# Kernel tuning notes

Measured on AMD Instinct MI355X. Metric: run time of the kernel, lower is better.

The kernel has to match this reference:

```python
import jax, jax.numpy as jnp
import numpy as np

M, N, P, T = 8000, 63, 64, 5


def setup_inputs() -> dict:
    key = jax.random.key(0)
    ks = jax.random.split(key, 19)
    sn = (1.0 / N) ** 0.5
    sp = (1.0 / P) ** 0.5
    f32 = jnp.float32
    return {
        "A": jax.random.normal(ks[0], (1, M, N), f32),
        "b": jax.random.normal(ks[1], (1, M), f32),
        "c": jax.random.normal(ks[2], (1, N), f32),
        "theta1r": sn * jax.random.normal(ks[3], (P, N + 1), f32),
        "theta1c": sn * jax.random.normal(ks[4], (P, N + 1), f32),
        "theta2rr": sp * jax.random.normal(ks[5], (P, P), f32),
        "theta2rc": sp * jax.random.normal(ks[6], (P, P), f32),
        "theta2cr": sp * jax.random.normal(ks[7], (P, P), f32),
        "theta3rr": sp * jax.random.normal(ks[8], (P, P), f32),
        "theta3rc": sp * jax.random.normal(ks[9], (P, P), f32),
        "theta3cr": sp * jax.random.normal(ks[10], (P, P), f32),
        "theta4rr": sp * jax.random.normal(ks[11], (P,), f32),
        "theta4rc": sp * jax.random.normal(ks[12], (P,), f32),
        "theta4cr": sp * jax.random.normal(ks[13], (P,), f32),
        "theta6r": sp * jax.random.normal(ks[14], (P, P), f32),
        "theta6c": sp * jax.random.normal(ks[15], (P, P), f32),
        "theta7": sp * jax.random.normal(ks[16], (P, P), f32),
        "W8": 0.05 * jax.random.normal(ks[17], (2, 2 * P), f32),
        "b8": 0.05 * jax.random.normal(ks[18], (2,), f32),
        "z": 7,
    }


def reference(A, b, c, theta1r, theta1c, theta2rr, theta2rc, theta2cr,
              theta3rr, theta3rc, theta3cr, theta4rr, theta4rc, theta4cr,
              theta6r, theta6c, theta7, W8, b8, z):
    relu = jax.nn.relu
    m, n = A.shape[1], A.shape[2]
    p = theta1r.shape[0]
    # raw node features: row node v -> [A[v,:], b[v]]; column node m -> [c, 0]
    Fr_raw = jnp.concatenate([A[0], b[0][:, None]], axis=1)        # (m, n+1)
    fc_raw = jnp.concatenate([c[0], jnp.zeros((1,), A.dtype)])     # (n+1,)
    Fr = Fr_raw / jnp.linalg.norm(Fr_raw, axis=1, keepdims=True)   # f(v), v < m
    fc = fc_raw / jnp.linalg.norm(fc_raw)                          # f(m)
    # edge weights w(v,u) = f(v).f(u) are detached in the original (float(...data))
    Frd = jax.lax.stop_gradient(Fr)
    fcd = jax.lax.stop_gradient(fc)
    Wrr = Frd @ Frd.T                                              # (m, m)
    dg = jnp.diagonal(Wrr)
    srr_pos = relu(Wrr).sum(axis=1) - relu(dg)                     # sum over u != v
    srr_neg = relu(-Wrr).sum(axis=1) - relu(-dg)
    wrc = Frd @ fcd                                                # (m,) = w(v, m)
    # identity: sum_u relu(t4 * w_u) = relu(t4) * sum_u relu(w_u) + relu(-t4) * sum_u relu(-w_u)
    Srr = relu(theta4rr)[:, None] * srr_pos[None, :] + relu(-theta4rr)[:, None] * srr_neg[None, :]
    Src = relu(theta4rc)[:, None] * relu(wrc)[None, :] + relu(-theta4rc)[:, None] * relu(-wrc)[None, :]
    scr = relu(theta4cr) * relu(wrc).sum() + relu(-theta4cr) * relu(-wrc).sum()
    edge_r = theta3rr @ Srr + theta3rc @ Src                       # (p, m), constant over t
    edge_c = theta3cr @ scr                                        # (p,)
    fz = Fr[z]                                                     # z < m: row node feature
    t1r = theta1r @ fz                                             # (p,)
    t1c = theta1c @ fz
    # mu init (p, m+1) = [[Ab^T, c0^T]; 0]; split into row columns / column node
    mu_r0 = jnp.zeros((p, m), A.dtype).at[: n + 1].set(Fr_raw.T)
    mu_c0 = jnp.zeros((p,), A.dtype).at[: n + 1].set(fc_raw)

    def step(carry, _):
        mu_r, mu_c = carry
        # row nodes: term2rr uses old mu[:, v]; term2rc uses old mu[:, m]
        new_r = relu(t1r[:, None] + theta2rr @ mu_r + (theta2rc @ mu_c)[:, None] + edge_r)
        # column node updated last within a sweep -> sees updated row embeddings
        new_c = relu(t1c + theta2cr @ new_r.sum(axis=1) + edge_c)
        return (new_r, new_c), None

    (mu_r, mu_c), _ = jax.lax.scan(step, (mu_r0, mu_c0), None, length=T)
    term6 = theta6r @ mu_r.sum(axis=1) + theta6c @ mu_c            # (p,)
    term7 = theta7 @ mu_r[:, z]                                    # (p,)
    feat = jax.nn.sigmoid(jnp.concatenate([term6, term7]))         # (2p,)
    return (feat @ W8.T + b8)[None, :]                             # (1, 2)
```

## Files before the change

kernel.cpp:

```cpp
#include <hip/hip_runtime.h>
#include <math.h>

typedef __attribute__((ext_vector_type(8))) short short8;
typedef __attribute__((ext_vector_type(4))) float f32x4;

#define WS_SPART 0
#define WS_GPART 262144
#define WS_WPART 294912
#define WS_CPART 295936
#define WS_T1R   336896
#define WS_T1C   336960
#define WS_AL    337024
#define WS_BE    337088
#define WS_GA    337152
#define WS_DE    337216
#define WS_ECP   337280
#define WS_ECN   337344
#define WS_W     337408
#define WS_MUZ   337472
#define WS_WSUM  337536
#define WS_RNORM 337600
#define WS_R2H   345792
#define WS_R2L   347840
#define WS_CNT   349888
#define WS_FH    380928
#define WS_FL    643072

#define NBLK 125

__device__ __forceinline__ float waveReduceSum(float v) {
#pragma unroll
    for (int m = 32; m >= 1; m >>= 1) v += __shfl_xor(v, m, 64);
    return v;
}
__device__ __forceinline__ unsigned short f2bf(float f) {
    unsigned int u = __float_as_uint(f);
    unsigned int r = (u + 0x7fffu + ((u >> 16) & 1u)) >> 16;
    return (unsigned short)r;
}
__device__ __forceinline__ float bf2f(unsigned short h) {
    return __uint_as_float(((unsigned int)h) << 16);
}

__device__ __forceinline__ float sum32_coherent(const float* base) {
    float v[32];
#pragma unroll
    for (int i = 0; i < 32; i++)
        asm volatile("global_load_dword %0, %1, off sc0 sc1"
                     : "=v"(v[i]) : "v"(base + i * 256));
    asm volatile("s_waitcnt vmcnt(0)" ::: "memory");
    __builtin_amdgcn_sched_barrier(0);
    float s = 0.f;
#pragma unroll
    for (int i = 0; i < 32; i++) s += v[i];
    return s;
}

__global__ __launch_bounds__(256) void k_fr(
    const float* __restrict__ A, const float* __restrict__ b, const float* __restrict__ c,
    const float* __restrict__ th1r, const float* __restrict__ th1c,
    const float* __restrict__ th2rr, const float* __restrict__ th2rc,
    const float* __restrict__ th3rr, const float* __restrict__ th3rc, const float* __restrict__ th3cr,
    const float* __restrict__ th4rr, const float* __restrict__ th4rc, const float* __restrict__ th4cr,
    const int* __restrict__ zp,
    unsigned short* __restrict__ Fh, unsigned short* __restrict__ Fl,
    unsigned short* __restrict__ R2H, unsigned short* __restrict__ R2L,
    float* __restrict__ ws)
{
    int tid = threadIdx.x, lane = tid & 63, wid = tid >> 6;

    if (blockIdx.x == 512) {
        __shared__ float fcraw[64], fz[64], sh4a[64], sh4b[64];
        int p = lane;
        int z = zp[0];
        float cv = (p < 63) ? c[p] : 0.f;
        fcraw[p] = cv;
        float av = (p < 63) ? A[z * 63 + p] : b[z];
        float s2 = waveReduceSum(av * av);
        fz[p] = av * rsqrtf(s2);
        __syncthreads();

        float t1 = 0.f, t2 = 0.f, w0 = 0.f;
#pragma unroll 8
        for (int k = 0; k < 64; k++) {
            t1 += th1r[p * 64 + k] * fz[k];
            t2 += th1c[p * 64 + k] * fz[k];
            w0 += th2rc[p * 64 + k] * fcraw[k];
        }
        ws[WS_T1R + p] = t1;
        ws[WS_T1C + p] = t2;
        ws[WS_W + p] = t1 + w0;

        sh4a[p] = th4rr[p];
        sh4b[p] = th4rc[p];
        __syncthreads();
        float a = 0.f, bb = 0.f, g = 0.f, d = 0.f;
#pragma unroll 8
        for (int k = 0; k < 64; k++) {
            float t4 = sh4a[k];
            a  += th3rr[p * 64 + k] * fmaxf(t4, 0.f);
            bb += th3rr[p * 64 + k] * fmaxf(-t4, 0.f);
            float t5 = sh4b[k];
            g  += th3rc[p * 64 + k] * fmaxf(t5, 0.f);
            d  += th3rc[p * 64 + k] * fmaxf(-t5, 0.f);
        }
        ws[WS_AL + p] = a; ws[WS_BE + p] = bb;
        ws[WS_GA + p] = g; ws[WS_DE + p] = d;
        __syncthreads();
        sh4a[p] = th4cr[p];
        __syncthreads();
        float e1 = 0.f, e2 = 0.f;
#pragma unroll 8
        for (int k = 0; k < 64; k++) {
            float t6 = sh4a[k];
            e1 += th3cr[p * 64 + k] * fmaxf(t6, 0.f);
            e2 += th3cr[p * 64 + k] * fmaxf(-t6, 0.f);
        }
        ws[WS_ECP + p] = e1; ws[WS_ECN + p] = e2;

        if (tid < 16) ((int*)(ws + WS_CNT))[tid] = 0;
        if (tid < 192) {
#pragma unroll
            for (int t5 = 0; t5 < 5; t5++)
                ws[WS_CPART + t5 * 8192 + 8000 + tid] = 0.f;
        }

#pragma unroll
        for (int i = 0; i < 16; i++) {
            int idx = tid * 16 + i;
            float f = th2rr[idx];
            unsigned short h = f2bf(f);
            R2H[idx] = h;
            R2L[idx] = f2bf(f - bf2f(h));
        }
        return;
    }

    __shared__ float gsh[64];
    __shared__ float wsh2[2];
    if (tid < 64) gsh[tid] = 0.f;
    if (tid < 2) wsh2[tid] = 0.f;
    __syncthreads();

    float cv = (lane < 63) ? c[lane] : 0.f;
    float cn2 = waveReduceSum(cv * cv);
    float fcnl = cv * rsqrtf(cn2);

    int r0 = blockIdx.x * 16 + wid * 4;
    float gl = 0.f, lp = 0.f, ln = 0.f;
#pragma unroll
    for (int i = 0; i < 4; i++) {
        int r = r0 + i;
        if (r < 8000) {
            float val = (lane < 63) ? A[r * 63 + lane] : b[r];
            float s2 = waveReduceSum(val * val);
            float f = val * rsqrtf(s2);
            unsigned short h = f2bf(f);
            Fh[r * 64 + lane] = h;
            Fl[r * 64 + lane] = f2bf(f - bf2f(h));
            gl += f;
            float w = waveReduceSum(f * fcnl);
            if (lane == 0) {
                ws[WS_RNORM + r] = sqrtf(s2);
                lp += fmaxf(w, 0.f); ln += fmaxf(-w, 0.f);
            }
        } else {
            Fh[r * 64 + lane] = 0;
            Fl[r * 64 + lane] = 0;
        }
    }
    atomicAdd(&gsh[lane], gl);
    if (lane == 0) { atomicAdd(&wsh2[0], lp); atomicAdd(&wsh2[1], ln); }
    __syncthreads();
    if (tid < 64) ws[WS_GPART + blockIdx.x * 64 + tid] = gsh[tid];
    if (tid == 64) ws[WS_WPART + blockIdx.x * 2 + 0] = wsh2[0];
    if (tid == 65) ws[WS_WPART + blockIdx.x * 2 + 1] = wsh2[1];
}

__global__ __launch_bounds__(256) void k_gram(
    const unsigned short* __restrict__ Fh, float* __restrict__ ws)
{
    int tid = threadIdx.x, lane = tid & 63, wid = tid >> 6;
    int m = lane & 15, quad = lane >> 4;
    int vbase = blockIdx.x * 256 + wid * 64;

    short8 AH[8];
#pragma unroll
    for (int pt = 0; pt < 4; pt++)
#pragma unroll
        for (int q = 0; q < 2; q++)
            AH[pt * 2 + q] = *(const short8*)(Fh + (vbase + pt * 16 + m) * 64 + q * 32 + quad * 8);

    float srr[16];
#pragma unroll
    for (int i = 0; i < 16; i++) srr[i] = 0.f;

    const int y = blockIdx.y;
    const int boff = m * 64 + quad * 8;
    short8 B0[2], B1[2];
#pragma unroll
    for (int q = 0; q < 2; q++)
        B0[q] = *(const short8*)(Fh + y * 16 * 64 + boff + q * 32);

#pragma unroll 1
    for (int k2 = 0; k2 < 8; k2++) {
        int jB1 = y + 32 * (2 * k2 + 1);
#pragma unroll
        for (int q = 0; q < 2; q++)
            B1[q] = *(const short8*)(Fh + jB1 * 16 * 64 + boff + q * 32);
#pragma unroll
        for (int pt = 0; pt < 4; pt++) {
            f32x4 a = {0.f, 0.f, 0.f, 0.f};
            a = __builtin_amdgcn_mfma_f32_16x16x32_bf16(AH[pt * 2 + 0], B0[0], a, 0, 0, 0);
            a = __builtin_amdgcn_mfma_f32_16x16x32_bf16(AH[pt * 2 + 1], B0[1], a, 0, 0, 0);
#pragma unroll
            for (int r = 0; r < 4; r++) srr[pt * 4 + r] += fmaxf(a[r], 0.f);
        }
        if (k2 < 7) {
            int jB0 = y + 32 * (2 * k2 + 2);
#pragma unroll
            for (int q = 0; q < 2; q++)
                B0[q] = *(const short8*)(Fh + jB0 * 16 * 64 + boff + q * 32);
        }
#pragma unroll
        for (int pt = 0; pt < 4; pt++) {
            f32x4 a = {0.f, 0.f, 0.f, 0.f};
            a = __builtin_amdgcn_mfma_f32_16x16x32_bf16(AH[pt * 2 + 0], B1[0], a, 0, 0, 0);
            a = __builtin_amdgcn_mfma_f32_16x16x32_bf16(AH[pt * 2 + 1], B1[1], a, 0, 0, 0);
#pragma unroll
            for (int r = 0; r < 4; r++) srr[pt * 4 + r] += fmaxf(a[r], 0.f);
        }
    }
#pragma unroll
    for (int pt = 0; pt < 4; pt++)
#pragma unroll
        for (int r = 0; r < 4; r++) {
            float s = srr[pt * 4 + r];
            s += __shfl_xor(s, 1, 64); s += __shfl_xor(s, 2, 64);
            s += __shfl_xor(s, 4, 64); s += __shfl_xor(s, 8, 64);
            if (m == 0)
                ws[WS_SPART + y * 8192 + vbase + pt * 16 + quad * 4 + r] = s;
        }
}

__global__ __launch_bounds__(256) void k_mu_fused(
    const float* __restrict__ c,
    const float* __restrict__ th2cr, const float* __restrict__ th2rc,
    const float* __restrict__ th6r, const float* __restrict__ th6c,
    const float* __restrict__ th7, const float* __restrict__ W8,
    const float* __restrict__ b8, const int* __restrict__ zp,
    float* __restrict__ ws,
    const unsigned short* __restrict__ Fh, const unsigned short* __restrict__ Fl,
    const unsigned short* __restrict__ R2H, const unsigned short* __restrict__ R2L,
    float* __restrict__ out)
{
    __shared__ float XF[64][68];
    __shared__ unsigned short UHT[64][72], ULT[64][72];
    __shared__ float red[256], colp[256];
    __shared__ __align__(16) float wS[64], alS[64], beS[64], gaS[64], deS[64];
    __shared__ float fcnS[64], gS[64], sprow[64];
    __shared__ __align__(16) float e4sh[256];
    __shared__ float Ssh[64], ysh[64], feat[128], muzS[64];

    int tid = threadIdx.x, lane = tid & 63, wid = tid >> 6;
    int m = lane & 15, quad = lane >> 4;
    int v0 = blockIdx.x * 64;
    int cw = wid * 16 + m;
    int v = v0 + cw;
    int z = zp[0];
    int* cnt = (int*)(ws + WS_CNT);

    short8 RH[8], RL[8];
#pragma unroll
    for (int pt = 0; pt < 4; pt++)
#pragma unroll
        for (int q = 0; q < 2; q++) {
            int off = (pt * 16 + m) * 64 + q * 32 + quad * 8;
            RH[pt * 2 + q] = *(const short8*)(R2H + off);
            RL[pt * 2 + q] = *(const short8*)(R2L + off);
        }

    if (wid == 0) {
        float cv = (lane < 63) ? c[lane] : 0.f;
        float cn2 = waveReduceSum(cv * cv);
        fcnS[lane] = cv * rsqrtf(cn2);
        wS[lane] = ws[WS_W + lane];
    } else if (wid == 1) {
        alS[lane] = ws[WS_AL + lane]; beS[lane] = ws[WS_BE + lane];
        float wp = 0.f;
#pragma unroll
        for (int k = 0; k < 8; k++) wp += ws[WS_WPART + (lane + 64 * k) * 2];
        wp = waveReduceSum(wp);
        if (lane == 0) ws[WS_WSUM] = wp;
    } else if (wid == 2) {
        gaS[lane] = ws[WS_GA + lane]; deS[lane] = ws[WS_DE + lane];
        float wn = 0.f;
#pragma unroll
        for (int k = 0; k < 8; k++) wn += ws[WS_WPART + (lane + 64 * k) * 2 + 1];
        wn = waveReduceSum(wn);
        if (lane == 0) ws[WS_WSUM + 1] = wn;
    }
    float gv = 0.f;
#pragma unroll 8
    for (int bb = 0; bb < 128; bb++) gv += ws[WS_GPART + (wid * 128 + bb) * 64 + lane];
    red[tid] = gv;
    __syncthreads();
    if (tid < 64) gS[tid] = red[tid] + red[64 + tid] + red[128 + tid] + red[192 + tid];
    __syncthreads();
    float sv = 0.f;
#pragma unroll
    for (int y = wid * 8; y < wid * 8 + 8; y++) sv += ws[WS_SPART + y * 8192 + v0 + lane];
    red[tid] = sv;
    __syncthreads();
    if (tid < 64) sprow[tid] = red[tid] + red[64 + tid] + red[128 + tid] + red[192 + tid];
    __syncthreads();

    for (int i2 = 0; i2 < 16; i2++) {
        int i = wid * 16 + i2;
        int vr = v0 + i;
        float fr = bf2f(Fh[vr * 64 + lane]) + bf2f(Fl[vr * 64 + lane]);
        float dw = waveReduceSum(fr * fcnS[lane]);
        float dg = waveReduceSum(fr * gS[lane]);
        if (lane == 0) {
            float spv = sprow[i];
            float4 ee;
            ee.x = spv - 1.0f;
            ee.y = spv - dg;
            ee.z = fmaxf(dw, 0.f);
            ee.w = fmaxf(-dw, 0.f);
            *(float4*)(&e4sh[i * 4]) = ee;
        }
        XF[i][lane] = fr * ws[WS_RNORM + vr];
    }
    __syncthreads();

    short8 BH[2], BL[2];
#pragma unroll
    for (int q = 0; q < 2; q++) {
        float4 f0 = *(const float4*)(&XF[cw][q * 32 + quad * 8]);
        float4 f1 = *(const float4*)(&XF[cw][q * 32 + quad * 8 + 4]);
        float xv[8] = {f0.x, f0.y, f0.z, f0.w, f1.x, f1.y, f1.z, f1.w};
        short8 H, L;
#pragma unroll
        for (int j = 0; j < 8; j++) {
            unsigned short h = f2bf(xv[j]);
            H[j] = (short)h;
            L[j] = (short)f2bf(xv[j] - bf2f(h));
        }
        BH[q] = H; BL[q] = L;
    }
    float4 e = *(const float4*)(&e4sh[cw * 4]);

    for (int t = 0; t < 5; t++) {
        if (t > 0) {
            red[tid] = sum32_coherent(ws + WS_CPART + (t - 1) * 8192 + wid * 64 + lane);
            __syncthreads();
            if (tid < 64) Ssh[tid] = red[tid] + red[64 + tid] + red[128 + tid] + red[192 + tid];
            __syncthreads();
            {
                int p = wid * 16 + m;
                float acc = 0.f;
                const float4* rowp = (const float4*)(th2cr + p * 64 + quad * 16);
#pragma unroll
                for (int kk = 0; kk < 4; kk++) {
                    float4 r4 = rowp[kk];
                    acc += r4.x * Ssh[quad * 16 + 4 * kk]     + r4.y * Ssh[quad * 16 + 4 * kk + 1]
                         + r4.z * Ssh[quad * 16 + 4 * kk + 2] + r4.w * Ssh[quad * 16 + 4 * kk + 3];
                }
                acc += __shfl_xor(acc, 16, 64);
                acc += __shfl_xor(acc, 32, 64);
                if (quad == 0)
                    ysh[p] = fmaxf(acc + ws[WS_T1C + p] + ws[WS_WSUM] * ws[WS_ECP + p]
                                   + ws[WS_WSUM + 1] * ws[WS_ECN + p], 0.f);
            }
            __syncthreads();
            {
                int p = wid * 16 + m;
                float acc = 0.f;
                const float4* rowp = (const float4*)(th2rc + p * 64 + quad * 16);
#pragma unroll
                for (int kk = 0; kk < 4; kk++) {
                    float4 r4 = rowp[kk];
                    acc += r4.x * ysh[quad * 16 + 4 * kk]     + r4.y * ysh[quad * 16 + 4 * kk + 1]
                         + r4.z * ysh[quad * 16 + 4 * kk + 2] + r4.w * ysh[quad * 16 + 4 * kk + 3];
                }
                acc += __shfl_xor(acc, 16, 64);
                acc += __shfl_xor(acc, 32, 64);
                if (quad == 0) wS[p] = acc + ws[WS_T1R + p];
            }
#pragma unroll
            for (int q = 0; q < 2; q++) {
                BH[q] = *(const short8*)(&UHT[cw][q * 32 + quad * 8]);
                BL[q] = *(const short8*)(&ULT[cw][q * 32 + quad * 8]);
            }
        }
        __syncthreads();

#pragma unroll
        for (int pt = 0; pt < 4; pt++) {
            f32x4 a = {0.f, 0.f, 0.f, 0.f};
#pragma unroll
            for (int q = 0; q < 2; q++) {
                a = __builtin_amdgcn_mfma_f32_16x16x32_bf16(RH[pt*2+q], BH[q], a, 0, 0, 0);
                a = __builtin_amdgcn_mfma_f32_16x16x32_bf16(RH[pt*2+q], BL[q], a, 0, 0, 0);
                a = __builtin_amdgcn_mfma_f32_16x16x32_bf16(RL[pt*2+q], BH[q], a, 0, 0, 0);
            }
            int pbase = pt * 16 + quad * 4;
            float4 w4 = *(const float4*)(wS + pbase);
            float4 a4 = *(const float4*)(alS + pbase);
            float4 b4 = *(const float4*)(beS + pbase);
            float4 g4 = *(const float4*)(gaS + pbase);
            float4 d4 = *(const float4*)(deS + pbase);
            float u0 = fmaxf(a[0] + w4.x + a4.x*e.x + b4.x*e.y + g4.x*e.z + d4.x*e.w, 0.f);
            float u1 = fmaxf(a[1] + w4.y + a4.y*e.x + b4.y*e.y + g4.y*e.z + d4.y*e.w, 0.f);
            float u2 = fmaxf(a[2] + w4.z + a4.z*e.x + b4.z*e.y + g4.z*e.z + d4.z*e.w, 0.f);
            float u3 = fmaxf(a[3] + w4.w + a4.w*e.x + b4.w*e.y + g4.w*e.z + d4.w*e.w, 0.f);
            if (t < 4) {
                ushort4 h4, l4;
                h4.x = f2bf(u0); l4.x = f2bf(u0 - bf2f(h4.x));
                h4.y = f2bf(u1); l4.y = f2bf(u1 - bf2f(h4.y));
                h4.z = f2bf(u2); l4.z = f2bf(u2 - bf2f(h4.z));
                h4.w = f2bf(u3); l4.w = f2bf(u3 - bf2f(h4.w));
                *(ushort4*)(&UHT[cw][pbase]) = h4;
                *(ushort4*)(&ULT[cw][pbase]) = l4;
            } else if (v == z) {
                __hip_atomic_store(&ws[WS_MUZ + pbase + 0], u0, __ATOMIC_RELAXED, __HIP_MEMORY_SCOPE_AGENT);
                __hip_atomic_store(&ws[WS_MUZ + pbase + 1], u1, __ATOMIC_RELAXED, __HIP_MEMORY_SCOPE_AGENT);
                __hip_atomic_store(&ws[WS_MUZ + pbase + 2], u2, __ATOMIC_RELAXED, __HIP_MEMORY_SCOPE_AGENT);
                __hip_atomic_store(&ws[WS_MUZ + pbase + 3], u3, __ATOMIC_RELAXED, __HIP_MEMORY_SCOPE_AGENT);
            }
            float c0 = u0, c1 = u1, c2 = u2, c3 = u3;
#pragma unroll
            for (int mm = 1; mm < 16; mm <<= 1) {
                c0 += __shfl_xor(c0, mm, 64);
                c1 += __shfl_xor(c1, mm, 64);
                c2 += __shfl_xor(c2, mm, 64);
                c3 += __shfl_xor(c3, mm, 64);
            }
            if (m == 0) {
                colp[wid * 64 + pbase + 0] = c0;
                colp[wid * 64 + pbase + 1] = c1;
                colp[wid * 64 + pbase + 2] = c2;
                colp[wid * 64 + pbase + 3] = c3;
            }
        }
        __syncthreads();
        if (tid < 64)
            __hip_atomic_store(&ws[WS_CPART + t * 8192 + blockIdx.x * 64 + tid],
                               colp[tid] + colp[64 + tid] + colp[128 + tid] + colp[192 + tid],
                               __ATOMIC_RELAXED, __HIP_MEMORY_SCOPE_AGENT);

        __syncthreads();
        if (tid == 0) {
            int old = __hip_atomic_fetch_add(&cnt[t], 1, __ATOMIC_RELAXED, __HIP_MEMORY_SCOPE_AGENT);
            if (old == NBLK - 1) {
                __hip_atomic_store(&cnt[8 + t], 1, __ATOMIC_RELAXED, __HIP_MEMORY_SCOPE_AGENT);
            } else {
                while (__hip_atomic_load(&cnt[8 + t], __ATOMIC_RELAXED, __HIP_MEMORY_SCOPE_AGENT) == 0)
                    __builtin_amdgcn_s_sleep(1);
            }
        }
        __syncthreads();
    }

    if (blockIdx.x != 0) return;

    red[tid] = sum32_coherent(ws + WS_CPART + 4 * 8192 + wid * 64 + lane);
    if (tid < 64) {
        float mz;
        asm volatile("global_load_dword %0, %1, off sc0 sc1"
                     : "=v"(mz) : "v"(ws + WS_MUZ + tid));
        asm volatile("s_waitcnt vmcnt(0)" ::: "memory");
        __builtin_amdgcn_sched_barrier(0);
        muzS[tid] = mz;
    }
    __syncthreads();
    if (tid < 64) Ssh[tid] = red[tid] + red[64 + tid] + red[128 + tid] + red[192 + tid];
    __syncthreads();
    int p = tid;
    if (p < 64) {
        float acc = ws[WS_T1C + p] + ws[WS_WSUM] * ws[WS_ECP + p]
                  + ws[WS_WSUM + 1] * ws[WS_ECN + p];
#pragma unroll 8
        for (int k = 0; k < 64; k++) acc += th2cr[p * 64 + k] * Ssh[k];
        ysh[p] = fmaxf(acc, 0.f);
    }
    __syncthreads();
    if (p < 64) {
        float t6 = 0.f, t7 = 0.f;
#pragma unroll 8
        for (int k = 0; k < 64; k++) {
            t6 += th6r[p * 64 + k] * Ssh[k] + th6c[p * 64 + k] * ysh[k];
            t7 += th7[p * 64 + k] * muzS[k];
        }
        feat[p] = 1.f / (1.f + expf(-t6));
        feat[64 + p] = 1.f / (1.f + expf(-t7));
    }
    __syncthreads();
    if (p < 2) {
        float o = b8[p];
        for (int i = 0; i < 128; i++) o += W8[p * 128 + i] * feat[i];
        out[p] = o;
    }
}

extern "C" void kernel_launch(void* const* d_in, const int* in_sizes, int n_in,
                              void* d_out, int out_size, void* d_ws, size_t ws_size,
                              hipStream_t stream) {
    (void)in_sizes; (void)n_in; (void)out_size; (void)ws_size;
    const float* A     = (const float*)d_in[0];
    const float* b     = (const float*)d_in[1];
    const float* c     = (const float*)d_in[2];
    const float* th1r  = (const float*)d_in[3];
    const float* th1c  = (const float*)d_in[4];
    const float* th2rr = (const float*)d_in[5];
    const float* th2rc = (const float*)d_in[6];
    const float* th2cr = (const float*)d_in[7];
    const float* th3rr = (const float*)d_in[8];
    const float* th3rc = (const float*)d_in[9];
    const float* th3cr = (const float*)d_in[10];
    const float* th4rr = (const float*)d_in[11];
    const float* th4rc = (const float*)d_in[12];
    const float* th4cr = (const float*)d_in[13];
    const float* th6r  = (const float*)d_in[14];
    const float* th6c  = (const float*)d_in[15];
    const float* th7   = (const float*)d_in[16];
    const float* W8    = (const float*)d_in[17];
    const float* b8    = (const float*)d_in[18];
    const int*   zp    = (const int*)d_in[19];
    float* ws  = (float*)d_ws;
    float* out = (float*)d_out;
    unsigned short* Fh  = (unsigned short*)(ws + WS_FH);
    unsigned short* Fl  = (unsigned short*)(ws + WS_FL);
    unsigned short* R2H = (unsigned short*)(ws + WS_R2H);
    unsigned short* R2L = (unsigned short*)(ws + WS_R2L);

    k_fr<<<513, 256, 0, stream>>>(A, b, c, th1r, th1c, th2rr, th2rc, th3rr, th3rc,
                                  th3cr, th4rr, th4rc, th4cr, zp, Fh, Fl, R2H, R2L, ws);
    k_gram<<<dim3(32, 32), 256, 0, stream>>>(Fh, ws);
    {
        const unsigned short* Fhc = Fh;
        const unsigned short* Flc = Fl;
        const unsigned short* R2Hc = R2H;
        const unsigned short* R2Lc = R2L;
        void* kargs[] = {
            (void*)&c, (void*)&th2cr, (void*)&th2rc, (void*)&th6r, (void*)&th6c,
            (void*)&th7, (void*)&W8, (void*)&b8, (void*)&zp, (void*)&ws,
            (void*)&Fhc, (void*)&Flc, (void*)&R2Hc, (void*)&R2Lc, (void*)&out };
        hipLaunchCooperativeKernel((const void*)k_mu_fused, dim3(NBLK), dim3(256),
                                   kargs, 0, stream);
    }
}
```

Measured before the change: 234.9 us.

## Replace counter barrier with per-block flags and overlap MFMA with barrier wait

Replaces the atomic counter plus release-flag grid barrier with per-block ready flags that waiting blocks poll with a single wave using coherent loads. The MFMA product theta2rr@mu for each step is moved ahead of the wait for the previous step's column partials, so tensor work overlaps the inter-block synchronisation. Block 0 now explicitly polls before the final reduction, and one reduction loop is unrolled further. This adds polling traffic over 128 flags per step and relies on correct memory ordering via an explicit waitcnt before the flag store.

New measurement: 227.4 us. -3.2%, faster.

```diff
diff --git a/kernel.cpp b/kernel.cpp
--- a/kernel.cpp
+++ b/kernel.cpp
@@ -22,7 +22,7 @@
 #define WS_RNORM 337600
 #define WS_R2H   345792
 #define WS_R2L   347840
-#define WS_CNT   349888
+#define WS_FLAG  349888
 #define WS_FH    380928
 #define WS_FL    643072
 
@@ -54,6 +54,20 @@
 #pragma unroll
     for (int i = 0; i < 32; i++) s += v[i];
     return s;
+}
+
+__device__ __forceinline__ void pollFlags(const int* fb, int lane) {
+    for (;;) {
+        int f0, f1;
+        asm volatile("global_load_dword %0, %1, off sc0 sc1"
+                     : "=v"(f0) : "v"(fb + lane));
+        asm volatile("global_load_dword %0, %1, off sc0 sc1"
+                     : "=v"(f1) : "v"(fb + 64 + lane));
+        asm volatile("s_waitcnt vmcnt(0)" : "+v"(f0), "+v"(f1) :: "memory");
+        __builtin_amdgcn_sched_barrier(0);
+        if (__all((f0 == 1) && (f1 == 1))) return;
+        __builtin_amdgcn_s_sleep(1);
+    }
 }
 
 __global__ __launch_bounds__(256) void k_fr(
@@ -118,7 +132,12 @@
         }
         ws[WS_ECP + p] = e1; ws[WS_ECN + p] = e2;
 
-        if (tid < 16) ((int*)(ws + WS_CNT))[tid] = 0;
+        if (tid < 128) {
+            int* fl = (int*)(ws + WS_FLAG);
+#pragma unroll
+            for (int t5 = 0; t5 < 5; t5++)
+                fl[t5 * 128 + tid] = (tid >= NBLK) ? 1 : 0;
+        }
         if (tid < 192) {
 #pragma unroll
             for (int t5 = 0; t5 < 5; t5++)
@@ -268,7 +287,7 @@
     int cw = wid * 16 + m;
     int v = v0 + cw;
     int z = zp[0];
-    int* cnt = (int*)(ws + WS_CNT);
+    int* flags = (int*)(ws + WS_FLAG);
 
     short8 RH[8], RL[8];
 #pragma unroll
@@ -301,7 +320,7 @@
         if (lane == 0) ws[WS_WSUM + 1] = wn;
     }
     float gv = 0.f;
-#pragma unroll 8
+#pragma unroll 32
     for (int bb = 0; bb < 128; bb++) gv += ws[WS_GPART + (wid * 128 + bb) * 64 + lane];
     red[tid] = gv;
     __syncthreads();
@@ -353,58 +372,69 @@
 
     for (int t = 0; t < 5; t++) {
         if (t > 0) {
+#pragma unroll
+            for (int q = 0; q < 2; q++) {
+                BH[q] = *(const short8*)(&UHT[cw][q * 32 + quad * 8]);
+                BL[q] = *(const short8*)(&ULT[cw][q * 32 + quad * 8]);
+            }
+        }
+        f32x4 acc[4];
+#pragma unroll
+        for (int pt = 0; pt < 4; pt++) {
+            f32x4 a = {0.f, 0.f, 0.f, 0.f};
+#pragma unroll
+            for (int q = 0; q < 2; q++) {
+                a = __builtin_amdgcn_mfma_f32_16x16x32_bf16(RH[pt*2+q], BH[q], a, 0, 0, 0);
+                a = __builtin_amdgcn_mfma_f32_16x16x32_bf16(RH[pt*2+q], BL[q], a, 0, 0, 0);
+                a = __builtin_amdgcn_mfma_f32_16x16x32_bf16(RL[pt*2+q], BH[q], a, 0, 0, 0);
+            }
+            acc[pt] = a;
+        }
+
+        if (t > 0) {
+            if (wid == 0) pollFlags(flags + (t - 1) * 128, lane);
+            __syncthreads();
             red[tid] = sum32_coherent(ws + WS_CPART + (t - 1) * 8192 + wid * 64 + lane);
             __syncthreads();
             if (tid < 64) Ssh[tid] = red[tid] + red[64 + tid] + red[128 + tid] + red[192 + tid];
             __syncthreads();
             {
                 int p = wid * 16 + m;
-                float acc = 0.f;
+                float acc2 = 0.f;
                 const float4* rowp = (const float4*)(th2cr + p * 64 + quad * 16);
 #pragma unroll
                 for (int kk = 0; kk < 4; kk++) {
                     float4 r4 = rowp[kk];
-                    acc += r4.x * Ssh[quad * 16 + 4 * kk]     + r4.y * Ssh[quad * 16 + 4 * kk + 1]
-                         + r4.z * Ssh[quad * 16 + 4 * kk + 2] + r4.w * Ssh[quad * 16 + 4 * kk + 3];
+                    acc2 += r4.x * Ssh[quad * 16 + 4 * kk]     + r4.y * Ssh[quad * 16 + 4 * kk + 1]
+                          + r4.z * Ssh[quad * 16 + 4 * kk + 2] + r4.w * Ssh[quad * 16 + 4 * kk + 3];
                 }
-                acc += __shfl_xor(acc, 16, 64);
-                acc += __shfl_xor(acc, 32, 64);
+                acc2 += __shfl_xor(acc2, 16, 64);
+                acc2 += __shfl_xor(acc2, 32, 64);
                 if (quad == 0)
-                    ysh[p] = fmaxf(acc + ws[WS_T1C + p] + ws[WS_WSUM] * ws[WS_ECP + p]
+                    ysh[p] = fmaxf(acc2 + ws[WS_T1C + p] + ws[WS_WSUM] * ws[WS_ECP + p]
                                    + ws[WS_WSUM + 1] * ws[WS_ECN + p], 0.f);
             }
             __syncthreads();
             {
                 int p = wid * 16 + m;
-                float acc = 0.f;
+                float acc2 = 0.f;
                 const float4* rowp = (const float4*)(th2rc + p * 64 + quad * 16);
 #pragma unroll
                 for (int kk = 0; kk < 4; kk++) {
                     float4 r4 = rowp[kk];
-                    acc += r4.x * ysh[quad * 16 + 4 * kk]     + r4.y * ysh[quad * 16 + 4 * kk + 1]
-                         + r4.z * ysh[quad * 16 + 4 * kk + 2] + r4.w * ysh[quad * 16 + 4 * kk + 3];
+                    acc2 += r4.x * ysh[quad * 16 + 4 * kk]     + r4.y * ysh[quad * 16 + 4 * kk + 1]
+                          + r4.z * ysh[quad * 16 + 4 * kk + 2] + r4.w * ysh[quad * 16 + 4 * kk + 3];
                 }
-                acc += __shfl_xor(acc, 16, 64);
-                acc += __shfl_xor(acc, 32, 64);
-                if (quad == 0) wS[p] = acc + ws[WS_T1R + p];
-            }
-#pragma unroll
-            for (int q = 0; q < 2; q++) {
-                BH[q] = *(const short8*)(&UHT[cw][q * 32 + quad * 8]);
-                BL[q] = *(const short8*)(&ULT[cw][q * 32 + quad * 8]);
-            }
-        }
-        __syncthreads();
+                acc2 += __shfl_xor(acc2, 16, 64);
+                acc2 += __shfl_xor(acc2, 32, 64);
+                if (quad == 0) wS[p] = acc2 + ws[WS_T1R + p];
+            }
+            __syncthreads();
+        }
 
 #pragma unroll
         for (int pt = 0; pt < 4; pt++) {
-            f32x4 a = {0.f, 0.f, 0.f, 0.f};
-#pragma unroll
-            for (int q = 0; q < 2; q++) {
-                a = __builtin_amdgcn_mfma_f32_16x16x32_bf16(RH[pt*2+q], BH[q], a, 0, 0, 0);
-                a = __builtin_amdgcn_mfma_f32_16x16x32_bf16(RH[pt*2+q], BL[q], a, 0, 0, 0);
-                a = __builtin_amdgcn_mfma_f32_16x16x32_bf16(RL[pt*2+q], BH[q], a, 0, 0, 0);
-            }
+            f32x4 a = acc[pt];
             int pbase = pt * 16 + quad * 4;
             float4 w4 = *(const float4*)(wS + pbase);
             float4 a4 = *(const float4*)(alS + pbase);
@@ -449,28 +479,25 @@
             __hip_atomic_store(&ws[WS_CPART + t * 8192 + blockIdx.x * 64 + tid],
                                colp[tid] + colp[64 + tid] + colp[128 + tid] + colp[192 + tid],
                                __ATOMIC_RELAXED, __HIP_MEMORY_SCOPE_AGENT);
-
         __syncthreads();
         if (tid == 0) {
-            int old = __hip_atomic_fetch_add(&cnt[t], 1, __ATOMIC_RELAXED, __HIP_MEMORY_SCOPE_AGENT);
-            if (old == NBLK - 1) {
-                __hip_atomic_store(&cnt[8 + t], 1, __ATOMIC_RELAXED, __HIP_MEMORY_SCOPE_AGENT);
-            } else {
-                while (__hip_atomic_load(&cnt[8 + t], __ATOMIC_RELAXED, __HIP_MEMORY_SCOPE_AGENT) == 0)
-                    __builtin_amdgcn_s_sleep(1);
-            }
-        }
-        __syncthreads();
+            asm volatile("s_waitcnt vmcnt(0)" ::: "memory");
+            __hip_atomic_store(&flags[t * 128 + (int)blockIdx.x], 1,
+                               __ATOMIC_RELAXED, __HIP_MEMORY_SCOPE_AGENT);
+        }
     }
 
     if (blockIdx.x != 0) return;
+
+    if (wid == 0) pollFlags(flags + 4 * 128, lane);
+    __syncthreads();
 
     red[tid] = sum32_coherent(ws + WS_CPART + 4 * 8192 + wid * 64 + lane);
     if (tid < 64) {
         float mz;
         asm volatile("global_load_dword %0, %1, off sc0 sc1"
                      : "=v"(mz) : "v"(ws + WS_MUZ + tid));
-        asm volatile("s_waitcnt vmcnt(0)" ::: "memory");
+        asm volatile("s_waitcnt vmcnt(0)" : "+v"(mz) :: "memory");
         __builtin_amdgcn_sched_barrier(0);
         muzS[tid] = mz;
     }
@@ -479,11 +506,11 @@
     __syncthreads();
     int p = tid;
     if (p < 64) {
-        float acc = ws[WS_T1C + p] + ws[WS_WSUM] * ws[WS_ECP + p]
-                  + ws[WS_WSUM + 1] * ws[WS_ECN + p];
+        float acc2 = ws[WS_T1C + p] + ws[WS_WSUM] * ws[WS_ECP + p]
+                   + ws[WS_WSUM + 1] * ws[WS_ECN + p];
 #pragma unroll 8
-        for (int k = 0; k < 64; k++) acc += th2cr[p * 64 + k] * Ssh[k];
-        ysh[p] = fmaxf(acc, 0.f);
+        for (int k = 0; k < 64; k++) acc2 += th2cr[p * 64 + k] * Ssh[k];
+        ysh[p] = fmaxf(acc2, 0.f);
     }
     __syncthreads();
     if (p < 64) {
```
